# Kernel tuning notes

Measured on AMD Instinct MI355X. Metric: run time of the kernel, lower is better.

## Reference

```python
import jax, jax.numpy as jnp
import numpy as np

KS = 3          # deform kernel size
N = KS * KS     # sampling points per output pixel
PAD = 1         # zero padding

def conv2d(x, w, stride, padding):
    return jax.lax.conv_general_dilated(
        x, w, (stride, stride), [(padding, padding), (padding, padding)],
        dimension_numbers=('NCHW', 'OIHW', 'NCHW'))

def _gather(x_flat, qx, qy, Wp):
    # x_flat: [b, c, Hp*Wp]; qx, qy: [b, h, w, N] int32 -> [b, c, h, w, N]
    b = qx.shape[0]; c = x_flat.shape[1]
    idx = (qx * Wp + qy).reshape(b, 1, -1)
    out = jnp.take_along_axis(x_flat, jnp.broadcast_to(idx, (b, c, idx.shape[-1])), axis=2)
    return out.reshape(b, c, qx.shape[1], qx.shape[2], qx.shape[3])

def deform_conv(x, w_off, b_off, w_conv):
    # learned per-pixel offsets: [b, 2N, h, w] (first N = x-offsets, last N = y-offsets)
    offset = conv2d(x, w_off, 1, PAD) + b_off[None, :, None, None]
    b, _, h, w = offset.shape
    x_pad = jnp.pad(x, ((0, 0), (0, 0), (PAD, PAD), (PAD, PAD)))
    Hp, Wp = x_pad.shape[2], x_pad.shape[3]
    # kernel-relative offsets p_n in {-1,0,1}^2
    pn_x, pn_y = jnp.meshgrid(jnp.arange(-(KS // 2), KS // 2 + 1),
                              jnp.arange(-(KS // 2), KS // 2 + 1), indexing='ij')
    p_n = jnp.concatenate([pn_x.reshape(-1), pn_y.reshape(-1)]).reshape(1, 2 * N, 1, 1)
    # base grid p_0 (1..h, 1..w in padded coordinates)
    p0_x, p0_y = jnp.meshgrid(jnp.arange(1, h + 1), jnp.arange(1, w + 1), indexing='ij')
    p_0 = jnp.concatenate([jnp.tile(p0_x[None], (N, 1, 1)),
                           jnp.tile(p0_y[None], (N, 1, 1))])[None]  # [1, 2N, h, w]
    p = (p_0 + p_n).astype(offset.dtype) + offset                   # [b, 2N, h, w]
    p = jnp.transpose(p, (0, 2, 3, 1))                              # [b, h, w, 2N]
    px, py = p[..., :N], p[..., N:]
    q = jnp.floor(jax.lax.stop_gradient(p))
    qlt_x = jnp.clip(q[..., :N], 0, Hp - 1); qlt_y = jnp.clip(q[..., N:], 0, Wp - 1)
    qrb_x = jnp.clip(q[..., :N] + 1, 0, Hp - 1); qrb_y = jnp.clip(q[..., N:] + 1, 0, Wp - 1)
    px = jnp.clip(px, 0, Hp - 1); py = jnp.clip(py, 0, Wp - 1)
    # bilinear weights (classic DCN formulation)
    g_lt = (1 + (qlt_x - px)) * (1 + (qlt_y - py))
    g_rb = (1 - (qrb_x - px)) * (1 - (qrb_y - py))
    g_lb = (1 + (qlt_x - px)) * (1 - (qrb_y - py))
    g_rt = (1 - (qrb_x - px)) * (1 + (qlt_y - py))
    x_flat = x_pad.reshape(b, x_pad.shape[1], -1)
    qi = lambda a: a.astype(jnp.int32)
    x_lt = _gather(x_flat, qi(qlt_x), qi(qlt_y), Wp)
    x_rb = _gather(x_flat, qi(qrb_x), qi(qrb_y), Wp)
    x_lb = _gather(x_flat, qi(qlt_x), qi(qrb_y), Wp)
    x_rt = _gather(x_flat, qi(qrb_x), qi(qlt_y), Wp)
    xo = (g_lt[:, None] * x_lt + g_rb[:, None] * x_rb
          + g_lb[:, None] * x_lb + g_rt[:, None] * x_rt)  # [b, c, h, w, N]
    c = xo.shape[1]
    # unfold N -> (ks, ks) blocks: [b, c, h*ks, w*ks]
    xo = xo.reshape(b, c, h, w, KS, KS).transpose(0, 1, 2, 4, 3, 5).reshape(b, c, h * KS, w * KS)
    return conv2d(xo, w_conv, KS, 0)  # stride=ks aggregation, no bias

def reference(x, w_off, b_off, w_conv, w_fc, b_fc):
    y = jax.nn.relu(deform_conv(x, w_off, b_off, w_conv))          # [b, 8, 28, 28]
    y = jax.lax.reduce_window(y, -jnp.inf, jax.lax.max,
                              (1, 1, 2, 2), (1, 1, 2, 2), 'VALID')  # [b, 8, 14, 14]
    y = y.reshape(y.shape[0], -1)
    return y @ w_fc.T + b_fc

def setup_inputs() -> dict:
    key = jax.random.key(0)
    k1, k2, k3, k4 = jax.random.split(key, 4)
    B = 4096
    return {
        'x': jax.random.normal(k1, (B, 1, 28, 28), dtype=jnp.float32),
        'w_off': jax.random.normal(k2, (18, 1, 3, 3), dtype=jnp.float32) * 0.1,
        'b_off': jnp.zeros((18,), dtype=jnp.float32),
        'w_conv': jax.random.normal(k3, (8, 1, 3, 3), dtype=jnp.float32) * 0.3,
        'w_fc': jax.random.normal(k4, (10, 8 * 14 * 14), dtype=jnp.float32) * 0.02,
        'b_fc': jnp.zeros((10,), dtype=jnp.float32),
    }
```

## Files before the change

### kernel.cpp

```cpp
#include <hip/hip_runtime.h>


#define HH 28
#define WW 28
#define WP 30
#define NPOS 784
#define NPOOL 1568
#define CELLS 196

__global__ __launch_bounds__(256) void deform_net_kernel(
    const float* __restrict__ x,
    const float* __restrict__ w_off,
    const float* __restrict__ b_off,
    const float* __restrict__ w_conv,
    const float* __restrict__ w_fc,
    const float* __restrict__ b_fc,
    float* __restrict__ out,
    int B)
{
    __shared__ float xs[3 * 900];
    __shared__ float wo_s[162];
    __shared__ float bo_s[18];
    __shared__ float wc_s[72];

    const int tid      = threadIdx.x;
    const int cell0    = blockIdx.x << 8;
    const int img_base = cell0 / CELLS;
    const int base_lc  = cell0 - img_base * CELLS;

    if (tid < 162) wo_s[tid] = w_off[tid];
    if (tid < 18)  bo_s[tid] = b_off[tid];
    if (tid < 72)  wc_s[tid] = w_conv[tid];

    for (int i = tid; i < 2700; i += 256) {
        int s = i / 900;
        int j = i - s * 900;
        int img = img_base + s;
        float v = 0.f;
        if (img < B) {
            int r = j / WP, c = j - r * WP;
            if (r >= 1 && r <= HH && c >= 1 && c <= WW)
                v = x[(size_t)img * NPOS + (r - 1) * WW + (c - 1)];
        }
        xs[i] = v;
    }
    __syncthreads();

    const int lc   = base_lc + tid;
    const int slot = (lc >= 2 * CELLS) ? 2 : (lc >= CELLS ? 1 : 0);
    const int cell = lc - slot * CELLS;
    const int xb0  = slot * 900;
    const bool act = (cell0 + tid) < B * CELLS;

    float fc[10];
    #pragma unroll
    for (int c = 0; c < 10; c++) fc[c] = 0.f;

    if (act) {
        const int ph = cell / 14, pw = cell % 14;
        const int h0 = 2 * ph, w0 = 2 * pw;

        float nb[16];
        #pragma unroll
        for (int i = 0; i < 4; i++)
            #pragma unroll
            for (int j = 0; j < 4; j++)
                nb[i * 4 + j] = xs[xb0 + (h0 + i) * WP + (w0 + j)];

        float acc[4][8];
        #pragma unroll
        for (int p = 0; p < 4; p++)
            #pragma unroll
            for (int o = 0; o < 8; o++) acc[p][o] = 0.f;

        #pragma unroll
        for (int k = 0; k < 9; k++) {
            const int kx = k / 3, ky = k % 3;
            #pragma unroll
            for (int p = 0; p < 4; p++) {
                const int dh = p >> 1, dw = p & 1;

                float offx = bo_s[k], offy = bo_s[k + 9];
                #pragma unroll
                for (int t = 0; t < 9; t++) {
                    float nv = nb[(dh + t / 3) * 4 + (dw + t % 3)];
                    offx = fmaf(wo_s[k * 9 + t],       nv, offx);
                    offy = fmaf(wo_s[(k + 9) * 9 + t], nv, offy);
                }

                float p_x = (float)(h0 + dh + kx) + offx;
                float p_y = (float)(w0 + dw + ky) + offy;

                float q0x = floorf(p_x), q0y = floorf(p_y);
                float qltx = fminf(fmaxf(q0x,       0.f), 29.f);
                float qlty = fminf(fmaxf(q0y,       0.f), 29.f);
                float qrbx = fminf(fmaxf(q0x + 1.f, 0.f), 29.f);
                float qrby = fminf(fmaxf(q0y + 1.f, 0.f), 29.f);
                float px   = fminf(fmaxf(p_x,       0.f), 29.f);
                float py   = fminf(fmaxf(p_y,       0.f), 29.f);

                float gltx = 1.f + (qltx - px);
                float glty = 1.f + (qlty - py);
                float grbx = 1.f - (qrbx - px);
                float grby = 1.f - (qrby - py);

                int ilx = (int)qltx, ily = (int)qlty;
                int irx = (int)qrbx, iry = (int)qrby;

                float xlt = xs[xb0 + ilx * WP + ily];
                float xrb = xs[xb0 + irx * WP + iry];
                float xlb = xs[xb0 + ilx * WP + iry];
                float xrt = xs[xb0 + irx * WP + ily];

                float s = gltx * (glty * xlt + grby * xlb)
                        + grbx * (glty * xrt + grby * xrb);

                #pragma unroll
                for (int o = 0; o < 8; o++)
                    acc[p][o] = fmaf(wc_s[o * 9 + k], s, acc[p][o]);
            }
        }

        #pragma unroll
        for (int o = 0; o < 8; o++) {
            float m = fmaxf(fmaxf(acc[0][o], acc[1][o]),
                            fmaxf(acc[2][o], acc[3][o]));
            m = fmaxf(m, 0.f);
            const float* wrow = w_fc + o * CELLS + cell;
            #pragma unroll
            for (int c = 0; c < 10; c++)
                fc[c] = fmaf(m, wrow[c * NPOOL], fc[c]);
        }
        if (cell == 0) {
            #pragma unroll
            for (int c = 0; c < 10; c++) fc[c] += b_fc[c];
        }
    }

    const int lane = tid & 63;
    const int wfl  = base_lc + (tid & ~63);
    const int s0   = (wfl >= 2 * CELLS) ? 2 : (wfl >= CELLS ? 1 : 0);
    const int wll  = wfl + 63;
    const int s1   = (wll >= 2 * CELLS) ? 2 : (wll >= CELLS ? 1 : 0);
    const int img0 = img_base + s0;
    const int img1 = img_base + s1;

    if (s0 == s1) {
        #pragma unroll
        for (int c = 0; c < 10; c++) {
            float v = fc[c];
            #pragma unroll
            for (int sh = 32; sh > 0; sh >>= 1) v += __shfl_down(v, sh, 64);
            if (lane == 0 && img0 < B) atomicAdd(&out[img0 * 10 + c], v);
        }
    } else {
        const bool in0 = (slot == s0);
        #pragma unroll
        for (int c = 0; c < 10; c++) {
            float v0 = in0 ? fc[c] : 0.f;
            float v1 = fc[c] - v0;
            #pragma unroll
            for (int sh = 32; sh > 0; sh >>= 1) {
                v0 += __shfl_down(v0, sh, 64);
                v1 += __shfl_down(v1, sh, 64);
            }
            if (lane == 0) {
                if (img0 < B) atomicAdd(&out[img0 * 10 + c], v0);
                if (img1 < B) atomicAdd(&out[img1 * 10 + c], v1);
            }
        }
    }
}

extern "C" void kernel_launch(void* const* d_in, const int* in_sizes, int n_in,
                              void* d_out, int out_size, void* d_ws, size_t ws_size,
                              hipStream_t stream) {
    const float* x      = (const float*)d_in[0];
    const float* w_off  = (const float*)d_in[1];
    const float* b_off  = (const float*)d_in[2];
    const float* w_conv = (const float*)d_in[3];
    const float* w_fc   = (const float*)d_in[4];
    const float* b_fc   = (const float*)d_in[5];
    float* out = (float*)d_out;

    const int B = in_sizes[0] / NPOS;
    const int grid = (B * CELLS + 255) / 256;

    hipMemsetAsync(d_out, 0, (size_t)out_size * sizeof(float), stream);
    deform_net_kernel<<<grid, 256, 0, stream>>>(x, w_off, b_off, w_conv,
                                                w_fc, b_fc, out, B);
}
```

Measured before the change: 144.2 us.

## Assign two whole images per block and reduce FC outputs in shared memory

Each block now handles exactly two images with 448 threads (392 active) instead of 256 cells that can straddle up to three images. The per-image FC partial sums are reduced through shared memory and written directly, so the global atomics and the separate memset launch are gone. Clamps are also switched to the med3 intrinsic. In exchange, 56 of the 448 threads do no sampling work and the shared input tile per block gets smaller.

```diff
diff --git a/kernel.cpp b/kernel.cpp
--- a/kernel.cpp
+++ b/kernel.cpp
@@ -7,8 +7,10 @@
 #define NPOS 784
 #define NPOOL 1568
 #define CELLS 196
+#define IPB 2
+#define NTHR 448
 
-__global__ __launch_bounds__(256) void deform_net_kernel(
+__global__ __launch_bounds__(NTHR) void deform_net_kernel(
     const float* __restrict__ x,
     const float* __restrict__ w_off,
     const float* __restrict__ b_off,
@@ -18,22 +20,21 @@
     float* __restrict__ out,
     int B)
 {
-    __shared__ float xs[3 * 900];
+    __shared__ float xs[IPB * 900];
     __shared__ float wo_s[162];
     __shared__ float bo_s[18];
     __shared__ float wc_s[72];
+    __shared__ float red[IPB][7][10];
 
     const int tid      = threadIdx.x;
-    const int cell0    = blockIdx.x << 8;
-    const int img_base = cell0 / CELLS;
-    const int base_lc  = cell0 - img_base * CELLS;
+    const int img_base = blockIdx.x * IPB;
 
     if (tid < 162) wo_s[tid] = w_off[tid];
     if (tid < 18)  bo_s[tid] = b_off[tid];
     if (tid < 72)  wc_s[tid] = w_conv[tid];
 
-    for (int i = tid; i < 2700; i += 256) {
-        int s = i / 900;
+    for (int i = tid; i < IPB * 900; i += NTHR) {
+        int s = (i >= 900) ? 1 : 0;
         int j = i - s * 900;
         int img = img_base + s;
         float v = 0.f;
@@ -46,17 +47,15 @@
     }
     __syncthreads();
 
-    const int lc   = base_lc + tid;
-    const int slot = (lc >= 2 * CELLS) ? 2 : (lc >= CELLS ? 1 : 0);
-    const int cell = lc - slot * CELLS;
-    const int xb0  = slot * 900;
-    const bool act = (cell0 + tid) < B * CELLS;
+    const int img_l = (tid >= CELLS) ? 1 : 0;
+    const int cell  = tid - img_l * CELLS;
+    const int xb0   = img_l * 900;
 
     float fc[10];
     #pragma unroll
     for (int c = 0; c < 10; c++) fc[c] = 0.f;
 
-    if (act) {
+    if (tid < IPB * CELLS && img_base + img_l < B) {
         const int ph = cell / 14, pw = cell % 14;
         const int h0 = 2 * ph, w0 = 2 * pw;
 
@@ -92,12 +91,12 @@
                 float p_y = (float)(w0 + dw + ky) + offy;
 
                 float q0x = floorf(p_x), q0y = floorf(p_y);
-                float qltx = fminf(fmaxf(q0x,       0.f), 29.f);
-                float qlty = fminf(fmaxf(q0y,       0.f), 29.f);
-                float qrbx = fminf(fmaxf(q0x + 1.f, 0.f), 29.f);
-                float qrby = fminf(fmaxf(q0y + 1.f, 0.f), 29.f);
-                float px   = fminf(fmaxf(p_x,       0.f), 29.f);
-                float py   = fminf(fmaxf(p_y,       0.f), 29.f);
+                float qltx = __builtin_amdgcn_fmed3f(q0x,       0.f, 29.f);
+                float qlty = __builtin_amdgcn_fmed3f(q0y,       0.f, 29.f);
+                float qrbx = __builtin_amdgcn_fmed3f(q0x + 1.f, 0.f, 29.f);
+                float qrby = __builtin_amdgcn_fmed3f(q0y + 1.f, 0.f, 29.f);
+                float px   = __builtin_amdgcn_fmed3f(p_x,       0.f, 29.f);
+                float py   = __builtin_amdgcn_fmed3f(p_y,       0.f, 29.f);
 
                 float gltx = 1.f + (qltx - px);
                 float glty = 1.f + (qlty - py);
@@ -138,23 +137,10 @@
     }
 
     const int lane = tid & 63;
-    const int wfl  = base_lc + (tid & ~63);
-    const int s0   = (wfl >= 2 * CELLS) ? 2 : (wfl >= CELLS ? 1 : 0);
-    const int wll  = wfl + 63;
-    const int s1   = (wll >= 2 * CELLS) ? 2 : (wll >= CELLS ? 1 : 0);
-    const int img0 = img_base + s0;
-    const int img1 = img_base + s1;
+    const int w    = tid >> 6;
 
-    if (s0 == s1) {
-        #pragma unroll
-        for (int c = 0; c < 10; c++) {
-            float v = fc[c];
-            #pragma unroll
-            for (int sh = 32; sh > 0; sh >>= 1) v += __shfl_down(v, sh, 64);
-            if (lane == 0 && img0 < B) atomicAdd(&out[img0 * 10 + c], v);
-        }
-    } else {
-        const bool in0 = (slot == s0);
+    if (w == 3) {
+        const bool in0 = (img_l == 0);
         #pragma unroll
         for (int c = 0; c < 10; c++) {
             float v0 = in0 ? fc[c] : 0.f;
@@ -165,9 +151,30 @@
                 v1 += __shfl_down(v1, sh, 64);
             }
             if (lane == 0) {
-                if (img0 < B) atomicAdd(&out[img0 * 10 + c], v0);
-                if (img1 < B) atomicAdd(&out[img1 * 10 + c], v1);
+                red[0][3][c] = v0;
+                red[1][3][c] = v1;
             }
+        }
+    } else {
+        const int seg = (w < 3) ? 0 : 1;
+        #pragma unroll
+        for (int c = 0; c < 10; c++) {
+            float v = fc[c];
+            #pragma unroll
+            for (int sh = 32; sh > 0; sh >>= 1) v += __shfl_down(v, sh, 64);
+            if (lane == 0) red[seg][w][c] = v;
+        }
+    }
+    __syncthreads();
+
+    if (tid < IPB * 10) {
+        int il = tid / 10, c = tid - il * 10;
+        int img = img_base + il;
+        if (img < B) {
+            int wlo = il ? 3 : 0;
+            float a = red[il][wlo][c] + red[il][wlo + 1][c]
+                    + red[il][wlo + 2][c] + red[il][wlo + 3][c];
+            out[img * 10 + c] = a;
         }
     }
 }
@@ -184,9 +191,7 @@
     float* out = (float*)d_out;
 
     const int B = in_sizes[0] / NPOS;
-    const int grid = (B * CELLS + 255) / 256;
-
-    hipMemsetAsync(d_out, 0, (size_t)out_size * sizeof(float), stream);
-    deform_net_kernel<<<grid, 256, 0, stream>>>(x, w_off, b_off, w_conv,
-                                                w_fc, b_fc, out, B);
+    const int grid = (B + IPB - 1) / IPB;
+    deform_net_kernel<<<grid, NTHR, 0, stream>>>(x, w_off, b_off, w_conv,
+                                                 w_fc, b_fc, out, B);
 }
```

New measurement: 140.4 us. -2.6%, faster.
